# Optimization experiments

Hardware: AMD Instinct MI355X
Metric: run time of the kernel (lower is better)

Reference implementation:

```python
import jax, jax.numpy as jnp
import numpy as np

N_NODES = 50000
D_FEAT = 128
N_EDGES = 600000
HIDDEN_1 = 128
HIDDEN_2 = 64


def setup_inputs() -> dict:
    key = jax.random.key(0)
    ks = jax.random.split(key, 8)
    features = jax.random.normal(ks[0], (N_NODES, D_FEAT), dtype=jnp.float32)
    edges = jax.random.randint(ks[1], (N_EDGES, 2), 0, N_NODES, dtype=jnp.int64)
    s1 = 1.0 / np.sqrt(D_FEAT)
    s2 = 1.0 / np.sqrt(2 * HIDDEN_1)
    s3 = 1.0 / np.sqrt(HIDDEN_2)
    return {
        "features": features,
        "edges": edges,
        "W_nb": jax.random.normal(ks[2], (D_FEAT, HIDDEN_1), dtype=jnp.float32) * s1,
        "b_nb": jnp.zeros((HIDDEN_1,), dtype=jnp.float32),
        "W_self": jax.random.normal(ks[3], (D_FEAT, HIDDEN_1), dtype=jnp.float32) * s1,
        "b_self": jnp.zeros((HIDDEN_1,), dtype=jnp.float32),
        "W_att1": jax.random.normal(ks[4], (2 * HIDDEN_1, HIDDEN_2), dtype=jnp.float32) * s2,
        "b_att1": jnp.zeros((HIDDEN_2,), dtype=jnp.float32),
        "W_att2": jax.random.normal(ks[5], (HIDDEN_2, 1), dtype=jnp.float32) * s3,
        "b_att2": jnp.zeros((1,), dtype=jnp.float32),
    }


def reference(features, edges, W_nb, b_nb, W_self, b_self, W_att1, b_att1, W_att2, b_att2):
    # gather endpoint node features for each edge: [E, D_FEAT]
    f1 = features[edges[:, 0]]
    f2 = features[edges[:, 1]]
    # per-endpoint dense projections with relu (inference: no dropout)
    h1 = jax.nn.relu(f1 @ W_nb + b_nb)      # [E, H1]
    h2 = jax.nn.relu(f2 @ W_self + b_self)  # [E, H1]
    h = jnp.concatenate([h1, h2], axis=1)   # [E, 2*H1]
    h = jax.nn.relu(h @ W_att1 + b_att1)    # [E, H2]
    weight = h @ W_att2 + b_att2            # [E, 1], linear output
    return weight
```

## Files before the change

kernel.cpp:

```cpp
#include <hip/hip_runtime.h>


#define N_NODES 50000
#define D_FEAT  128
#define H1      128
#define H2      64
#define N_EDGES 600000

typedef unsigned short u16;
typedef __attribute__((ext_vector_type(8))) short bf16x8;
typedef __attribute__((ext_vector_type(4))) float f32x4;

union FragU { uint4 u; bf16x8 v; };

static __device__ __forceinline__ unsigned bfpack(float a, float b) {
    union { float f; unsigned u; } x, y; x.f = a; y.f = b;
    unsigned lo = (x.u + 0x7fffu + ((x.u >> 16) & 1u)) >> 16;
    unsigned hi = (y.u + 0x7fffu + ((y.u >> 16) & 1u)) & 0xffff0000u;
    return lo | hi;
}
static __device__ __forceinline__ u16 f2bf(float f) {
    union { float f; unsigned u; } v; v.f = f;
    return (u16)((v.u + 0x7fffu + ((v.u >> 16) & 1u)) >> 16);
}
static __device__ __forceinline__ float bflo(unsigned u) {
    union { unsigned u; float f; } v; v.u = u << 16; return v.f;
}
static __device__ __forceinline__ float bfhi(unsigned u) {
    union { unsigned u; float f; } v; v.u = u & 0xffff0000u; return v.f;
}

__global__ __launch_bounds__(256) void node_kernel(
    const float* __restrict__ feat,
    const float* __restrict__ Wnb,  const float* __restrict__ bnb,
    const float* __restrict__ Wsf,  const float* __restrict__ bsf,
    const float* __restrict__ Wat1, const float* __restrict__ bat1,
    u16* __restrict__ a1, u16* __restrict__ a2)
{
    __shared__ u16 Abuf[4 * 4 * 64 * 8];
    __shared__ u16 Hbuf[4 * 8 * 64 * 8];

    const int t    = threadIdx.x;
    const int w    = t >> 6;
    const int lane = t & 63;
    const int m    = lane & 15;
    const int q    = lane >> 4;
    const int n0   = blockIdx.x * 64;

    #pragma unroll
    for (int s = 0; s < 8; ++s) {
        const int i   = s * 256 + t;
        const int row = i >> 5;
        const int c4  = i & 31;
        const int gn  = n0 + row;
        float4 v = make_float4(0.f, 0.f, 0.f, 0.f);
        if (gn < N_NODES)
            v = *((const float4*)(feat + (size_t)gn * D_FEAT + c4 * 4));
        const int k0  = c4 * 4;
        const int kc  = k0 >> 5;
        const int qq  = (k0 >> 3) & 3;
        const int j0  = k0 & 7;
        const int idx = (((row >> 4) * 4 + kc) * 64 + (qq * 16 + (row & 15))) * 8 + j0;
        uint2 p; p.x = bfpack(v.x, v.y); p.y = bfpack(v.z, v.w);
        *((uint2*)&Abuf[idx]) = p;
    }

    FragU w1f[4][4];
    #pragma unroll
    for (int ms = 0; ms < 4; ++ms) {
        const int col = w * 64 + ms * 16 + m;
        const float* src = (col < H1) ? (Wnb + col) : (Wsf + (col - H1));
        #pragma unroll
        for (int kc = 0; kc < 4; ++kc) {
            const int k0 = kc * 32 + q * 8;
            float e[8];
            #pragma unroll
            for (int j = 0; j < 8; ++j) e[j] = src[(size_t)(k0 + j) * H1];
            w1f[ms][kc].u = make_uint4(bfpack(e[0], e[1]), bfpack(e[2], e[3]),
                                       bfpack(e[4], e[5]), bfpack(e[6], e[7]));
        }
    }

    f32x4 acc1[4][4];
    #pragma unroll
    for (int i = 0; i < 4; ++i)
        #pragma unroll
        for (int j = 0; j < 4; ++j)
            acc1[i][j] = (f32x4){0.f, 0.f, 0.f, 0.f};

    __syncthreads();

    #pragma unroll
    for (int kc = 0; kc < 4; ++kc) {
        #pragma unroll
        for (int ns = 0; ns < 4; ++ns) {
            FragU ff; ff.u = *((const uint4*)&Abuf[((ns * 4 + kc) * 64 + lane) * 8]);
            #pragma unroll
            for (int ms = 0; ms < 4; ++ms)
                acc1[ms][ns] = __builtin_amdgcn_mfma_f32_16x16x32_bf16(
                    w1f[ms][kc].v, ff.v, acc1[ms][ns], 0, 0, 0);
        }
    }

    #pragma unroll
    for (int ms = 0; ms < 4; ++ms) {
        const int hcol0 = w * 64 + ms * 16 + q * 4;
        const float* bsrc = (hcol0 < H1) ? (bnb + hcol0) : (bsf + (hcol0 - H1));
        const float4 bb = *((const float4*)bsrc);
        const int kc2 = hcol0 >> 5;
        const int q2  = (hcol0 >> 3) & 3;
        const int j0  = hcol0 & 7;
        #pragma unroll
        for (int ns = 0; ns < 4; ++ns) {
            const f32x4 a = acc1[ms][ns];
            const float v0 = fmaxf(a.x + bb.x, 0.f);
            const float v1 = fmaxf(a.y + bb.y, 0.f);
            const float v2 = fmaxf(a.z + bb.z, 0.f);
            const float v3 = fmaxf(a.w + bb.w, 0.f);
            const int idx = ((ns * 8 + kc2) * 64 + (q2 * 16 + m)) * 8 + j0;
            uint2 p; p.x = bfpack(v0, v1); p.y = bfpack(v2, v3);
            *((uint2*)&Hbuf[idx]) = p;
        }
    }

    const int kbase = (w < 2) ? 0 : H1;
    FragU w2f[2][4];
    #pragma unroll
    for (int ns2 = 0; ns2 < 2; ++ns2) {
        const int col2 = (w & 1) * 32 + ns2 * 16 + m;
        #pragma unroll
        for (int kc = 0; kc < 4; ++kc) {
            const int k0 = kbase + kc * 32 + q * 8;
            float e[8];
            #pragma unroll
            for (int j = 0; j < 8; ++j) e[j] = Wat1[(size_t)(k0 + j) * H2 + col2];
            w2f[ns2][kc].u = make_uint4(bfpack(e[0], e[1]), bfpack(e[2], e[3]),
                                        bfpack(e[4], e[5]), bfpack(e[6], e[7]));
        }
    }

    f32x4 acc2[4][2];
    #pragma unroll
    for (int i = 0; i < 4; ++i) { acc2[i][0] = (f32x4){0.f,0.f,0.f,0.f};
                                  acc2[i][1] = (f32x4){0.f,0.f,0.f,0.f}; }

    __syncthreads();

    #pragma unroll
    for (int kc = 0; kc < 4; ++kc) {
        const int kc2 = kc + ((w < 2) ? 0 : 4);
        #pragma unroll
        for (int ms = 0; ms < 4; ++ms) {
            FragU hf; hf.u = *((const uint4*)&Hbuf[((ms * 8 + kc2) * 64 + lane) * 8]);
            #pragma unroll
            for (int ns2 = 0; ns2 < 2; ++ns2)
                acc2[ms][ns2] = __builtin_amdgcn_mfma_f32_16x16x32_bf16(
                    hf.v, w2f[ns2][kc].v, acc2[ms][ns2], 0, 0, 0);
        }
    }

    u16* aout = (w < 2) ? a1 : a2;
    #pragma unroll
    for (int ns2 = 0; ns2 < 2; ++ns2) {
        const int col2 = (w & 1) * 32 + ns2 * 16 + m;
        const float b2 = (w < 2) ? bat1[col2] : 0.f;
        #pragma unroll
        for (int ms = 0; ms < 4; ++ms) {
            const f32x4 a = acc2[ms][ns2];
            const int gn0 = n0 + ms * 16 + q * 4;
            if (gn0 + 0 < N_NODES) aout[(size_t)(gn0 + 0) * H2 + col2] = f2bf(a.x + b2);
            if (gn0 + 1 < N_NODES) aout[(size_t)(gn0 + 1) * H2 + col2] = f2bf(a.y + b2);
            if (gn0 + 2 < N_NODES) aout[(size_t)(gn0 + 2) * H2 + col2] = f2bf(a.z + b2);
            if (gn0 + 3 < N_NODES) aout[(size_t)(gn0 + 3) * H2 + col2] = f2bf(a.w + b2);
        }
    }
}

__global__ __launch_bounds__(256) void edge_kernel(
    const int* __restrict__ edges,
    const u16* __restrict__ a1, const u16* __restrict__ a2,
    const float* __restrict__ Wat2, const float* __restrict__ bat2,
    float* __restrict__ out)
{
    const int t  = threadIdx.x;
    const int l  = t & 7;
    const int g  = t >> 3;
    const int e0 = blockIdx.x * 64 + g;
    const int e1 = e0 + 32;

    const float4 w0 = ((const float4*)Wat2)[l * 2 + 0];
    const float4 w1 = ((const float4*)Wat2)[l * 2 + 1];
    const float  bias = bat2[0];

    const int2 pa = ((const int2*)edges)[e0];
    const int2 pb = ((const int2*)edges)[e1];
    const uint4 qa1 = ((const uint4*)(a1 + (size_t)pa.x * H2))[l];
    const uint4 qa2 = ((const uint4*)(a2 + (size_t)pa.y * H2))[l];
    const uint4 qb1 = ((const uint4*)(a1 + (size_t)pb.x * H2))[l];
    const uint4 qb2 = ((const uint4*)(a2 + (size_t)pb.y * H2))[l];

    float sa = 0.f, sb = 0.f;
    sa += fmaxf(bflo(qa1.x) + bflo(qa2.x), 0.f) * w0.x;
    sa += fmaxf(bfhi(qa1.x) + bfhi(qa2.x), 0.f) * w0.y;
    sa += fmaxf(bflo(qa1.y) + bflo(qa2.y), 0.f) * w0.z;
    sa += fmaxf(bfhi(qa1.y) + bfhi(qa2.y), 0.f) * w0.w;
    sa += fmaxf(bflo(qa1.z) + bflo(qa2.z), 0.f) * w1.x;
    sa += fmaxf(bfhi(qa1.z) + bfhi(qa2.z), 0.f) * w1.y;
    sa += fmaxf(bflo(qa1.w) + bflo(qa2.w), 0.f) * w1.z;
    sa += fmaxf(bfhi(qa1.w) + bfhi(qa2.w), 0.f) * w1.w;

    sb += fmaxf(bflo(qb1.x) + bflo(qb2.x), 0.f) * w0.x;
    sb += fmaxf(bfhi(qb1.x) + bfhi(qb2.x), 0.f) * w0.y;
    sb += fmaxf(bflo(qb1.y) + bflo(qb2.y), 0.f) * w0.z;
    sb += fmaxf(bfhi(qb1.y) + bfhi(qb2.y), 0.f) * w0.w;
    sb += fmaxf(bflo(qb1.z) + bflo(qb2.z), 0.f) * w1.x;
    sb += fmaxf(bfhi(qb1.z) + bfhi(qb2.z), 0.f) * w1.y;
    sb += fmaxf(bflo(qb1.w) + bflo(qb2.w), 0.f) * w1.z;
    sb += fmaxf(bfhi(qb1.w) + bfhi(qb2.w), 0.f) * w1.w;

    sa += __shfl_down(sa, 4, 8); sb += __shfl_down(sb, 4, 8);
    sa += __shfl_down(sa, 2, 8); sb += __shfl_down(sb, 2, 8);
    sa += __shfl_down(sa, 1, 8); sb += __shfl_down(sb, 1, 8);

    if (l == 0) { out[e0] = sa + bias; out[e1] = sb + bias; }
}

extern "C" void kernel_launch(void* const* d_in, const int* in_sizes, int n_in,
                              void* d_out, int out_size, void* d_ws, size_t ws_size,
                              hipStream_t stream) {
    const float* feat  = (const float*)d_in[0];
    const int*   edges = (const int*)d_in[1];
    const float* Wnb   = (const float*)d_in[2];
    const float* bnb   = (const float*)d_in[3];
    const float* Wsf   = (const float*)d_in[4];
    const float* bsf   = (const float*)d_in[5];
    const float* Wat1  = (const float*)d_in[6];
    const float* bat1  = (const float*)d_in[7];
    const float* Wat2  = (const float*)d_in[8];
    const float* bat2  = (const float*)d_in[9];
    float* out = (float*)d_out;

    u16* a1 = (u16*)d_ws;
    u16* a2 = a1 + (size_t)N_NODES * H2;

    const int node_blocks = (N_NODES + 63) / 64;
    node_kernel<<<node_blocks, 256, 0, stream>>>(feat, Wnb, bnb, Wsf, bsf,
                                                 Wat1, bat1, a1, a2);

    const int edge_blocks = N_EDGES / 64;
    edge_kernel<<<edge_blocks, 256, 0, stream>>>(edges, a1, a2, Wat2, bat2, out);
}
```

Baseline: 128.8 us.

## Prepack weights into MFMA fragment layout once; vectorize node stores; batch edges per thread

Adds a small prep kernel that converts the projection and attention weights to bf16 fragment-ordered buffers, so each node block loads them with uint4 reads instead of strided scalar fp32 loads plus conversion. The second MFMA swaps operand order, which lets each lane write four contiguous bf16 outputs for one node as one ushort4 store. The edge kernel now handles four edges per 8-lane group, giving more gathers in flight per thread. The cost is an extra kernel launch and added workspace use.

```diff
diff --git a/kernel.cpp b/kernel.cpp
--- a/kernel.cpp
+++ b/kernel.cpp
@@ -30,11 +30,47 @@
     union { unsigned u; float f; } v; v.u = u & 0xffff0000u; return v.f;
 }
 
+__global__ __launch_bounds__(256) void prep_kernel(
+    const float* __restrict__ Wnb, const float* __restrict__ Wsf,
+    const float* __restrict__ Wat1,
+    u16* __restrict__ W1F, u16* __restrict__ W2F)
+{
+    const int t = threadIdx.x;
+    const int b = blockIdx.x;
+    if (b < 16) {
+        const int cs = b;
+        const int kc = t >> 6, q = (t >> 4) & 3, m = t & 15;
+        const int col = cs * 16 + m;
+        const float* src = (col < H1) ? (Wnb + col) : (Wsf + (col - H1));
+        const int k0 = kc * 32 + q * 8;
+        float e[8];
+        #pragma unroll
+        for (int j = 0; j < 8; ++j) e[j] = src[(size_t)(k0 + j) * H1];
+        uint4 pk = make_uint4(bfpack(e[0], e[1]), bfpack(e[2], e[3]),
+                              bfpack(e[4], e[5]), bfpack(e[6], e[7]));
+        *((uint4*)&W1F[((cs * 4 + kc) * 64 + q * 16 + m) * 8]) = pk;
+    } else {
+        for (int i = t; i < 4 * 8 * 64; i += 256) {
+            const int lane = i & 63, pair = i >> 6;
+            const int kc = pair & 7, cs2 = pair >> 3;
+            const int q = lane >> 4, m = lane & 15;
+            const int col2 = cs2 * 16 + m;
+            const int k0 = kc * 32 + q * 8;
+            float e[8];
+            #pragma unroll
+            for (int j = 0; j < 8; ++j) e[j] = Wat1[(size_t)(k0 + j) * H2 + col2];
+            uint4 pk = make_uint4(bfpack(e[0], e[1]), bfpack(e[2], e[3]),
+                                  bfpack(e[4], e[5]), bfpack(e[6], e[7]));
+            *((uint4*)&W2F[(pair * 64 + lane) * 8]) = pk;
+        }
+    }
+}
+
 __global__ __launch_bounds__(256) void node_kernel(
     const float* __restrict__ feat,
-    const float* __restrict__ Wnb,  const float* __restrict__ bnb,
-    const float* __restrict__ Wsf,  const float* __restrict__ bsf,
-    const float* __restrict__ Wat1, const float* __restrict__ bat1,
+    const u16* __restrict__ W1F,  const u16* __restrict__ W2F,
+    const float* __restrict__ bnb,  const float* __restrict__ bsf,
+    const float* __restrict__ bat1,
     u16* __restrict__ a1, u16* __restrict__ a2)
 {
     __shared__ u16 Abuf[4 * 4 * 64 * 8];
@@ -46,6 +82,13 @@
     const int m    = lane & 15;
     const int q    = lane >> 4;
     const int n0   = blockIdx.x * 64;
+
+    FragU w1f[4][4];
+    #pragma unroll
+    for (int ms = 0; ms < 4; ++ms)
+        #pragma unroll
+        for (int kc = 0; kc < 4; ++kc)
+            w1f[ms][kc].u = *((const uint4*)&W1F[(((w * 4 + ms) * 4 + kc) * 64 + lane) * 8]);
 
     #pragma unroll
     for (int s = 0; s < 8; ++s) {
@@ -65,22 +108,6 @@
         *((uint2*)&Abuf[idx]) = p;
     }
 
-    FragU w1f[4][4];
-    #pragma unroll
-    for (int ms = 0; ms < 4; ++ms) {
-        const int col = w * 64 + ms * 16 + m;
-        const float* src = (col < H1) ? (Wnb + col) : (Wsf + (col - H1));
-        #pragma unroll
-        for (int kc = 0; kc < 4; ++kc) {
-            const int k0 = kc * 32 + q * 8;
-            float e[8];
-            #pragma unroll
-            for (int j = 0; j < 8; ++j) e[j] = src[(size_t)(k0 + j) * H1];
-            w1f[ms][kc].u = make_uint4(bfpack(e[0], e[1]), bfpack(e[2], e[3]),
-                                       bfpack(e[4], e[5]), bfpack(e[6], e[7]));
-        }
-    }
-
     f32x4 acc1[4][4];
     #pragma unroll
     for (int i = 0; i < 4; ++i)
@@ -123,19 +150,14 @@
         }
     }
 
-    const int kbase = (w < 2) ? 0 : H1;
     FragU w2f[2][4];
     #pragma unroll
     for (int ns2 = 0; ns2 < 2; ++ns2) {
-        const int col2 = (w & 1) * 32 + ns2 * 16 + m;
-        #pragma unroll
-        for (int kc = 0; kc < 4; ++kc) {
-            const int k0 = kbase + kc * 32 + q * 8;
-            float e[8];
-            #pragma unroll
-            for (int j = 0; j < 8; ++j) e[j] = Wat1[(size_t)(k0 + j) * H2 + col2];
-            w2f[ns2][kc].u = make_uint4(bfpack(e[0], e[1]), bfpack(e[2], e[3]),
-                                        bfpack(e[4], e[5]), bfpack(e[6], e[7]));
+        const int cs2 = (w & 1) * 2 + ns2;
+        #pragma unroll
+        for (int kcl = 0; kcl < 4; ++kcl) {
+            const int kc = kcl + ((w < 2) ? 0 : 4);
+            w2f[ns2][kcl].u = *((const uint4*)&W2F[((cs2 * 8 + kc) * 64 + lane) * 8]);
         }
     }
 
@@ -147,33 +169,51 @@
     __syncthreads();
 
     #pragma unroll
-    for (int kc = 0; kc < 4; ++kc) {
-        const int kc2 = kc + ((w < 2) ? 0 : 4);
+    for (int kcl = 0; kcl < 4; ++kcl) {
+        const int kc2 = kcl + ((w < 2) ? 0 : 4);
         #pragma unroll
         for (int ms = 0; ms < 4; ++ms) {
             FragU hf; hf.u = *((const uint4*)&Hbuf[((ms * 8 + kc2) * 64 + lane) * 8]);
             #pragma unroll
             for (int ns2 = 0; ns2 < 2; ++ns2)
                 acc2[ms][ns2] = __builtin_amdgcn_mfma_f32_16x16x32_bf16(
-                    hf.v, w2f[ns2][kc].v, acc2[ms][ns2], 0, 0, 0);
+                    w2f[ns2][kcl].v, hf.v, acc2[ms][ns2], 0, 0, 0);
         }
     }
 
     u16* aout = (w < 2) ? a1 : a2;
+    const int colbase = (w & 1) * 32;
     #pragma unroll
     for (int ns2 = 0; ns2 < 2; ++ns2) {
-        const int col2 = (w & 1) * 32 + ns2 * 16 + m;
-        const float b2 = (w < 2) ? bat1[col2] : 0.f;
+        const int c0 = colbase + ns2 * 16 + q * 4;
+        float4 b2 = make_float4(0.f, 0.f, 0.f, 0.f);
+        if (w < 2) b2 = *((const float4*)(bat1 + c0));
         #pragma unroll
         for (int ms = 0; ms < 4; ++ms) {
-            const f32x4 a = acc2[ms][ns2];
-            const int gn0 = n0 + ms * 16 + q * 4;
-            if (gn0 + 0 < N_NODES) aout[(size_t)(gn0 + 0) * H2 + col2] = f2bf(a.x + b2);
-            if (gn0 + 1 < N_NODES) aout[(size_t)(gn0 + 1) * H2 + col2] = f2bf(a.y + b2);
-            if (gn0 + 2 < N_NODES) aout[(size_t)(gn0 + 2) * H2 + col2] = f2bf(a.z + b2);
-            if (gn0 + 3 < N_NODES) aout[(size_t)(gn0 + 3) * H2 + col2] = f2bf(a.w + b2);
-        }
-    }
+            const int node = n0 + ms * 16 + m;
+            if (node < N_NODES) {
+                const f32x4 a = acc2[ms][ns2];
+                ushort4 pk;
+                pk.x = f2bf(a.x + b2.x); pk.y = f2bf(a.y + b2.y);
+                pk.z = f2bf(a.z + b2.z); pk.w = f2bf(a.w + b2.w);
+                *((ushort4*)(aout + (size_t)node * H2 + c0)) = pk;
+            }
+        }
+    }
+}
+
+static __device__ __forceinline__ float edot(uint4 q1, uint4 q2,
+                                             float4 w0, float4 w1) {
+    float s = 0.f;
+    s += fmaxf(bflo(q1.x) + bflo(q2.x), 0.f) * w0.x;
+    s += fmaxf(bfhi(q1.x) + bfhi(q2.x), 0.f) * w0.y;
+    s += fmaxf(bflo(q1.y) + bflo(q2.y), 0.f) * w0.z;
+    s += fmaxf(bfhi(q1.y) + bfhi(q2.y), 0.f) * w0.w;
+    s += fmaxf(bflo(q1.z) + bflo(q2.z), 0.f) * w1.x;
+    s += fmaxf(bfhi(q1.z) + bfhi(q2.z), 0.f) * w1.y;
+    s += fmaxf(bflo(q1.w) + bflo(q2.w), 0.f) * w1.z;
+    s += fmaxf(bfhi(q1.w) + bfhi(q2.w), 0.f) * w1.w;
+    return s;
 }
 
 __global__ __launch_bounds__(256) void edge_kernel(
@@ -182,47 +222,44 @@
     const float* __restrict__ Wat2, const float* __restrict__ bat2,
     float* __restrict__ out)
 {
-    const int t  = threadIdx.x;
-    const int l  = t & 7;
-    const int g  = t >> 3;
-    const int e0 = blockIdx.x * 64 + g;
-    const int e1 = e0 + 32;
+    const int t = threadIdx.x;
+    const int l = t & 7;
+    const int g = t >> 3;
+    const int base = blockIdx.x * 128 + g;
 
     const float4 w0 = ((const float4*)Wat2)[l * 2 + 0];
     const float4 w1 = ((const float4*)Wat2)[l * 2 + 1];
     const float  bias = bat2[0];
 
-    const int2 pa = ((const int2*)edges)[e0];
-    const int2 pb = ((const int2*)edges)[e1];
-    const uint4 qa1 = ((const uint4*)(a1 + (size_t)pa.x * H2))[l];
-    const uint4 qa2 = ((const uint4*)(a2 + (size_t)pa.y * H2))[l];
-    const uint4 qb1 = ((const uint4*)(a1 + (size_t)pb.x * H2))[l];
-    const uint4 qb2 = ((const uint4*)(a2 + (size_t)pb.y * H2))[l];
-
-    float sa = 0.f, sb = 0.f;
-    sa += fmaxf(bflo(qa1.x) + bflo(qa2.x), 0.f) * w0.x;
-    sa += fmaxf(bfhi(qa1.x) + bfhi(qa2.x), 0.f) * w0.y;
-    sa += fmaxf(bflo(qa1.y) + bflo(qa2.y), 0.f) * w0.z;
-    sa += fmaxf(bfhi(qa1.y) + bfhi(qa2.y), 0.f) * w0.w;
-    sa += fmaxf(bflo(qa1.z) + bflo(qa2.z), 0.f) * w1.x;
-    sa += fmaxf(bfhi(qa1.z) + bfhi(qa2.z), 0.f) * w1.y;
-    sa += fmaxf(bflo(qa1.w) + bflo(qa2.w), 0.f) * w1.z;
-    sa += fmaxf(bfhi(qa1.w) + bfhi(qa2.w), 0.f) * w1.w;
-
-    sb += fmaxf(bflo(qb1.x) + bflo(qb2.x), 0.f) * w0.x;
-    sb += fmaxf(bfhi(qb1.x) + bfhi(qb2.x), 0.f) * w0.y;
-    sb += fmaxf(bflo(qb1.y) + bflo(qb2.y), 0.f) * w0.z;
-    sb += fmaxf(bfhi(qb1.y) + bfhi(qb2.y), 0.f) * w0.w;
-    sb += fmaxf(bflo(qb1.z) + bflo(qb2.z), 0.f) * w1.x;
-    sb += fmaxf(bfhi(qb1.z) + bfhi(qb2.z), 0.f) * w1.y;
-    sb += fmaxf(bflo(qb1.w) + bflo(qb2.w), 0.f) * w1.z;
-    sb += fmaxf(bfhi(qb1.w) + bfhi(qb2.w), 0.f) * w1.w;
-
-    sa += __shfl_down(sa, 4, 8); sb += __shfl_down(sb, 4, 8);
-    sa += __shfl_down(sa, 2, 8); sb += __shfl_down(sb, 2, 8);
-    sa += __shfl_down(sa, 1, 8); sb += __shfl_down(sb, 1, 8);
-
-    if (l == 0) { out[e0] = sa + bias; out[e1] = sb + bias; }
+    int  e[4]; bool v[4]; int2 ep[4];
+    #pragma unroll
+    for (int i = 0; i < 4; ++i) {
+        e[i] = base + i * 32;
+        v[i] = e[i] < N_EDGES;
+        ep[i] = v[i] ? ((const int2*)edges)[e[i]] : make_int2(0, 0);
+    }
+
+    uint4 q1[4], q2[4];
+    #pragma unroll
+    for (int i = 0; i < 4; ++i) {
+        q1[i] = ((const uint4*)(a1 + (size_t)ep[i].x * H2))[l];
+        q2[i] = ((const uint4*)(a2 + (size_t)ep[i].y * H2))[l];
+    }
+
+    float s[4];
+    #pragma unroll
+    for (int i = 0; i < 4; ++i) {
+        s[i] = edot(q1[i], q2[i], w0, w1);
+        s[i] += __shfl_down(s[i], 4, 8);
+        s[i] += __shfl_down(s[i], 2, 8);
+        s[i] += __shfl_down(s[i], 1, 8);
+    }
+
+    if (l == 0) {
+        #pragma unroll
+        for (int i = 0; i < 4; ++i)
+            if (v[i]) out[e[i]] = s[i] + bias;
+    }
 }
 
 extern "C" void kernel_launch(void* const* d_in, const int* in_sizes, int n_in,
@@ -240,13 +277,17 @@
     const float* bat2  = (const float*)d_in[9];
     float* out = (float*)d_out;
 
-    u16* a1 = (u16*)d_ws;
-    u16* a2 = a1 + (size_t)N_NODES * H2;
+    u16* a1  = (u16*)d_ws;
+    u16* a2  = a1 + (size_t)N_NODES * H2;
+    u16* W1F = a2 + (size_t)N_NODES * H2;
+    u16* W2F = W1F + 16 * 4 * 64 * 8;
+
+    prep_kernel<<<17, 256, 0, stream>>>(Wnb, Wsf, Wat1, W1F, W2F);
 
     const int node_blocks = (N_NODES + 63) / 64;
-    node_kernel<<<node_blocks, 256, 0, stream>>>(feat, Wnb, bnb, Wsf, bsf,
-                                                 Wat1, bat1, a1, a2);
-
-    const int edge_blocks = N_EDGES / 64;
+    node_kernel<<<node_blocks, 256, 0, stream>>>(feat, W1F, W2F,
+                                                 bnb, bsf, bat1, a1, a2);
+
+    const int edge_blocks = (N_EDGES + 127) / 128;
     edge_kernel<<<edge_blocks, 256, 0, stream>>>(edges, a1, a2, Wat2, bat2, out);
 }
```

Measured after the change: 125.8 us. 1.02x faster.
